# Optimization experiments

Measured on AMD Instinct MI355X. Metric: run time of the kernel, lower is better.

Reference implementation:

```python
import jax, jax.numpy as jnp
import numpy as np
from functools import partial
from jax.scipy.special import gammaln, logsumexp

PAD_ID = 1
REG_1 = 0.02
REG_2 = 0.1
_J = 64  # series terms for log I_v(k); ample for k ~ sqrt(D), v = D/2 - 1


def _log_iv(v, k):
    # log of modified Bessel I_v(k) via its power series, evaluated in log-space:
    # I_v(k) = sum_j (k/2)^(2j+v) / (j! * Gamma(v+j+1))
    j = jnp.arange(_J, dtype=k.dtype)
    log_half_k = jnp.log(k * 0.5)[..., None]                      # [..., 1]
    log_terms = (2.0 * j + v) * log_half_k - gammaln(j + 1.0) - gammaln(v + j + 1.0)
    return logsumexp(log_terms, axis=-1)                          # [...]


@partial(jax.custom_vjp, nondiff_argnums=(0,))
def logcmk(m, k):
    # Faithful to LogCMK.forward: uses scipy-style ive => value = log C_m(k) + k
    v = m / 2.0 - 1.0
    log_ive = _log_iv(v, k) - k                                   # log(I_v(k) e^{-k})
    return v * jnp.log(k) - log_ive - (m / 2.0) * jnp.log(2.0 * jnp.pi)


def _logcmk_fwd(m, k):
    return logcmk(m, k), k


def _logcmk_bwd(m, k, g):
    # Faithful to LogCMK.backward: d/dk = -I_{m/2}(k) / I_{m/2-1}(k)
    v = m / 2.0 - 1.0
    ratio = jnp.exp(_log_iv(v + 1.0, k) - _log_iv(v, k))
    return (-ratio * g,)


logcmk.defvjp(_logcmk_fwd, _logcmk_bwd)


def setup_inputs() -> dict:
    key = jax.random.key(0)
    k1, k2, k3 = jax.random.split(key, 3)
    B, S, D, V = 32, 1024, 256, 50000
    preds = jax.random.normal(k1, (B, D, S), dtype=jnp.float32)
    emb_table = jax.random.normal(k2, (V, D), dtype=jnp.float32)
    # pretrained target embeddings are unit-norm direction vectors for vMF
    emb_table = emb_table / jnp.linalg.norm(emb_table, axis=1, keepdims=True)
    target = jax.random.randint(k3, (B, S), 0, V, dtype=jnp.int64)
    return {"preds": preds, "emb_table": emb_table, "target": target}


def reference(preds, emb_table, target):
    m = float(emb_table.shape[1])
    target_emb = emb_table[target]                        # [B, S, D] gather
    norm = jnp.linalg.norm(preds, axis=1)                 # [B, S]
    dot = jnp.einsum('bsd,bds->bs', target_emb, preds)    # [B, S]
    loss = -logcmk(m, norm) - REG_2 * dot + REG_1 * norm  # [B, S]
    mask = (target != PAD_ID).astype(loss.dtype)
    return jnp.sum(loss * mask) / jnp.sum(mask)
```

## Files before the change

### kernel.cpp

```cpp
#include <hip/hip_runtime.h>
#include <math.h>


constexpr int Dc = 256;
constexpr int Sc = 1024;
constexpr int Bc = 32;
constexpr int TILE = 64;
constexpr int NBLK = Bc * Sc / TILE;
constexpr int NW   = 8;

using f4 = __attribute__((ext_vector_type(4))) float;

__global__ __launch_bounds__(512, 4) void nllvmf_main(
    const float* __restrict__ preds,
    const float* __restrict__ emb,
    const int*   __restrict__ target,
    float*       __restrict__ partial)
{
    __shared__ float s_r[NW][2][64];

    const int tid = threadIdx.x;
    const int blk = blockIdx.x;
    const int b   = blk >> 4;
    const int s0  = (blk & 15) * TILE;
    const int w   = tid >> 6;
    const int l   = tid & 63;
    const int td  = l >> 3;
    const int sg  = l & 7;
    const int d0  = w * 32 + td * 4;
    const int p0  = s0 + sg * 4;

    const int4 tA = *reinterpret_cast<const int4*>(target + b * Sc + p0);
    const int4 tB = *reinterpret_cast<const int4*>(target + b * Sc + p0 + 32);
    const int tg[8] = {tA.x, tA.y, tA.z, tA.w, tB.x, tB.y, tB.z, tB.w};

    const float* pb = preds + (size_t)b * Dc * Sc + (size_t)d0 * Sc + p0;
    f4 p[4][2];
    #pragma unroll
    for (int q = 0; q < 4; ++q) {
        p[q][0] = __builtin_nontemporal_load(reinterpret_cast<const f4*>(pb + (size_t)q * Sc));
        p[q][1] = __builtin_nontemporal_load(reinterpret_cast<const f4*>(pb + (size_t)q * Sc + 32));
    }
    f4 e[8];
    #pragma unroll
    for (int j = 0; j < 8; ++j)
        e[j] = *reinterpret_cast<const f4*>(emb + (size_t)tg[j] * Dc + d0);

    float n2[8] = {0,0,0,0,0,0,0,0};
    float dt[8] = {0,0,0,0,0,0,0,0};
    #pragma unroll
    for (int q = 0; q < 4; ++q)
        #pragma unroll
        for (int j = 0; j < 8; ++j) {
            const float pv = p[q][j >> 2][j & 3];
            n2[j] = fmaf(pv, pv, n2[j]);
            dt[j] = fmaf(pv, e[j][q], dt[j]);
        }

    #pragma unroll
    for (int m = 8; m <= 32; m <<= 1)
        #pragma unroll
        for (int j = 0; j < 8; ++j) {
            n2[j] += __shfl_xor(n2[j], m, 64);
            dt[j] += __shfl_xor(dt[j], m, 64);
        }

    if (td == 0) {
        #pragma unroll
        for (int j = 0; j < 8; ++j) {
            const int pos = (j >> 2) * 32 + sg * 4 + (j & 3);
            s_r[w][0][pos] = n2[j];
            s_r[w][1][pos] = dt[j];
        }
    }
    __syncthreads();

    if (tid < 64) {
        float norm2 = 0.f, dot = 0.f;
        #pragma unroll
        for (int w2 = 0; w2 < NW; ++w2) {
            norm2 += s_r[w2][0][tid];
            dot   += s_r[w2][1][tid];
        }
        const int tgt = target[b * Sc + s0 + tid];

        const float k = sqrtf(norm2);
        const float r = 0.25f * norm2;

        constexpr float INV[32] = {
            1.0f/128.0f,  1.0f/258.0f,  1.0f/390.0f,  1.0f/524.0f,
            1.0f/660.0f,  1.0f/798.0f,  1.0f/938.0f,  1.0f/1080.0f,
            1.0f/1224.0f, 1.0f/1370.0f, 1.0f/1518.0f, 1.0f/1668.0f,
            1.0f/1820.0f, 1.0f/1974.0f, 1.0f/2130.0f, 1.0f/2288.0f,
            1.0f/2448.0f, 1.0f/2610.0f, 1.0f/2774.0f, 1.0f/2940.0f,
            1.0f/3108.0f, 1.0f/3278.0f, 1.0f/3450.0f, 1.0f/3624.0f,
            1.0f/3800.0f, 1.0f/3978.0f, 1.0f/4158.0f, 1.0f/4340.0f,
            1.0f/4524.0f, 1.0f/4710.0f, 1.0f/4898.0f, 1.0f/5088.0f };
        float t = 1.0f, S = 1.0f;
        #pragma unroll
        for (int j = 0; j < 32; ++j) { t *= r * INV[j]; S += t; }

        float loss = __logf(S) - 0.98f * k - 0.1f * dot - 344.3348757f;
        float msk  = (tgt != 1) ? 1.0f : 0.0f;
        loss *= msk;

        #pragma unroll
        for (int m = 32; m; m >>= 1) {
            loss += __shfl_xor(loss, m, 64);
            msk  += __shfl_xor(msk,  m, 64);
        }
        if (tid == 0) {
            partial[blk]        = loss;
            partial[NBLK + blk] = msk;
        }
    }
}

__global__ __launch_bounds__(128) void nllvmf_finalize(
    const float* __restrict__ partial, float* __restrict__ out)
{
    __shared__ float sl[2], sm[2];
    const int tid = threadIdx.x;
    f4 lv = *reinterpret_cast<const f4*>(partial + tid * 4);
    f4 mv = *reinterpret_cast<const f4*>(partial + NBLK + tid * 4);
    float l = lv.x + lv.y + lv.z + lv.w;
    float m = mv.x + mv.y + mv.z + mv.w;
    #pragma unroll
    for (int off = 32; off; off >>= 1) {
        l += __shfl_down(l, off, 64);
        m += __shfl_down(m, off, 64);
    }
    if ((tid & 63) == 0) { sl[tid >> 6] = l; sm[tid >> 6] = m; }
    __syncthreads();
    if (tid == 0)
        out[0] = (sl[0] + sl[1]) / (sm[0] + sm[1]);
}

extern "C" void kernel_launch(void* const* d_in, const int* in_sizes, int n_in,
                              void* d_out, int out_size, void* d_ws, size_t ws_size,
                              hipStream_t stream) {
    const float* preds  = (const float*)d_in[0];
    const float* emb    = (const float*)d_in[1];
    const int*   target = (const int*)d_in[2];
    float* out = (float*)d_out;
    float* ws  = (float*)d_ws;

    nllvmf_main<<<NBLK, 512, 0, stream>>>(preds, emb, target, ws);
    nllvmf_finalize<<<1, 128, 0, stream>>>(ws, out);
}
```

Measured before the change: 17.95 us.

## Fuse finalize reduction into main kernel via last-block atomic counter

```diff
diff --git a/kernel.cpp b/kernel.cpp
--- a/kernel.cpp
+++ b/kernel.cpp
@@ -11,13 +11,15 @@
 
 using f4 = __attribute__((ext_vector_type(4))) float;
 
-__global__ __launch_bounds__(512, 4) void nllvmf_main(
+__global__ __launch_bounds__(512, 4) void nllvmf_fused(
     const float* __restrict__ preds,
     const float* __restrict__ emb,
     const int*   __restrict__ target,
-    float*       __restrict__ partial)
+    float*       __restrict__ out,
+    float*       __restrict__ ws)
 {
     __shared__ float s_r[NW][2][64];
+    __shared__ int s_last;
 
     const int tid = threadIdx.x;
     const int blk = blockIdx.x;
@@ -38,8 +40,8 @@
     f4 p[4][2];
     #pragma unroll
     for (int q = 0; q < 4; ++q) {
-        p[q][0] = __builtin_nontemporal_load(reinterpret_cast<const f4*>(pb + (size_t)q * Sc));
-        p[q][1] = __builtin_nontemporal_load(reinterpret_cast<const f4*>(pb + (size_t)q * Sc + 32));
+        p[q][0] = *reinterpret_cast<const f4*>(pb + (size_t)q * Sc);
+        p[q][1] = *reinterpret_cast<const f4*>(pb + (size_t)q * Sc + 32);
     }
     f4 e[8];
     #pragma unroll
@@ -110,30 +112,29 @@
             msk  += __shfl_xor(msk,  m, 64);
         }
         if (tid == 0) {
-            partial[blk]        = loss;
-            partial[NBLK + blk] = msk;
+            __hip_atomic_store(&ws[blk],        loss, __ATOMIC_RELAXED, __HIP_MEMORY_SCOPE_AGENT);
+            __hip_atomic_store(&ws[NBLK + blk], msk,  __ATOMIC_RELAXED, __HIP_MEMORY_SCOPE_AGENT);
+            unsigned prev = __hip_atomic_fetch_add(
+                (unsigned*)(ws + 2 * NBLK), 1u, __ATOMIC_ACQ_REL, __HIP_MEMORY_SCOPE_AGENT);
+            s_last = (prev == (unsigned)(NBLK - 1));
         }
     }
-}
+    __syncthreads();
 
-__global__ __launch_bounds__(128) void nllvmf_finalize(
-    const float* __restrict__ partial, float* __restrict__ out)
-{
-    __shared__ float sl[2], sm[2];
-    const int tid = threadIdx.x;
-    f4 lv = *reinterpret_cast<const f4*>(partial + tid * 4);
-    f4 mv = *reinterpret_cast<const f4*>(partial + NBLK + tid * 4);
-    float l = lv.x + lv.y + lv.z + lv.w;
-    float m = mv.x + mv.y + mv.z + mv.w;
-    #pragma unroll
-    for (int off = 32; off; off >>= 1) {
-        l += __shfl_down(l, off, 64);
-        m += __shfl_down(m, off, 64);
+    if (s_last && tid < 64) {
+        float lsum = 0.f, msum = 0.f;
+        #pragma unroll
+        for (int i = tid; i < NBLK; i += 64) {
+            lsum += __hip_atomic_load(&ws[i],        __ATOMIC_RELAXED, __HIP_MEMORY_SCOPE_AGENT);
+            msum += __hip_atomic_load(&ws[NBLK + i], __ATOMIC_RELAXED, __HIP_MEMORY_SCOPE_AGENT);
+        }
+        #pragma unroll
+        for (int m = 32; m; m >>= 1) {
+            lsum += __shfl_xor(lsum, m, 64);
+            msum += __shfl_xor(msum, m, 64);
+        }
+        if (tid == 0) out[0] = lsum / msum;
     }
-    if ((tid & 63) == 0) { sl[tid >> 6] = l; sm[tid >> 6] = m; }
-    __syncthreads();
-    if (tid == 0)
-        out[0] = (sl[0] + sl[1]) / (sm[0] + sm[1]);
 }
 
 extern "C" void kernel_launch(void* const* d_in, const int* in_sizes, int n_in,
@@ -145,6 +146,6 @@
     float* out = (float*)d_out;
     float* ws  = (float*)d_ws;
 
-    nllvmf_main<<<NBLK, 512, 0, stream>>>(preds, emb, target, ws);
-    nllvmf_finalize<<<1, 128, 0, stream>>>(ws, out);
+    hipMemsetAsync(ws + 2 * NBLK, 0, sizeof(unsigned), stream);
+    nllvmf_fused<<<NBLK, 512, 0, stream>>>(preds, emb, target, out, ws);
 }
```

Result: slower. 34.68 us (+93.2%).
